# Performance work log

Hardware: AMD Instinct MI355X
Metric: run time of the kernel (lower is better)

Reference implementation:

```python
import jax, jax.numpy as jnp
import numpy as np
import math

B, T, C = 4, 2048, 1024
H, D = 16, 64            # num_heads, head_dim
ORIG_LEN = 4096
MIN_FREQ, MAX_FREQ = 0.5, 40.0


def setup_inputs() -> dict:
    key = jax.random.key(0)
    ks = jax.random.split(key, 6)
    x = jax.random.normal(ks[0], (B, T, C), dtype=jnp.float32)
    keep_idx = jnp.sort(jax.random.randint(ks[1], (B, T, 1), 0, ORIG_LEN), axis=1)
    W_qkv = jax.random.normal(ks[2], (C, 3 * C), dtype=jnp.float32) * (1.0 / math.sqrt(C))
    b_qkv = jnp.zeros((3 * C,), dtype=jnp.float32)
    W_proj = jax.random.normal(ks[3], (C, C), dtype=jnp.float32) * (1.0 / math.sqrt(C))
    b_proj = jnp.zeros((C,), dtype=jnp.float32)
    return {"x": x, "keep_idx": keep_idx, "original_seq_len": ORIG_LEN,
            "W_qkv": W_qkv, "b_qkv": b_qkv, "W_proj": W_proj, "b_proj": b_proj}


def _rope_angles(positions, orig_len):
    # positions: [b, t] float token positions in the ORIGINAL sequence.
    # golden_gate 1-D RoPE: normalized positions times geometric frequency band.
    half = D // 2
    freqs = MIN_FREQ * (MAX_FREQ / MIN_FREQ) ** (jnp.arange(half, dtype=jnp.float32) / (half - 1))
    pos_norm = positions / jnp.float32(orig_len)          # [b, t]
    return 2.0 * jnp.pi * pos_norm[:, :, None] * freqs    # [b, t, half]


def _apply_rope(x, cos, sin):
    # x: [b, h, t, d]; cos/sin: [b, 1, t, d/2]; rotate (first half, second half) pairs
    half = D // 2
    x1, x2 = x[..., :half], x[..., half:]
    return jnp.concatenate([x1 * cos - x2 * sin, x1 * sin + x2 * cos], axis=-1)


def reference(x, keep_idx, original_seq_len, W_qkv, b_qkv, W_proj, b_proj):
    b, t, c = x.shape
    # fused QKV projection + head split: (b,t,3c) -> (b,t,3,h,d) -> (b,h,t,3,d)
    qkv = (x @ W_qkv + b_qkv).reshape(b, t, 3, H, D).transpose(0, 3, 1, 2, 4)
    q, k, v = qkv[:, :, :, 0], qkv[:, :, :, 1], qkv[:, :, :, 2]  # each [b,h,t,d]

    positions = keep_idx[..., 0].astype(jnp.float32)             # [b, t]
    ang = _rope_angles(positions, original_seq_len)              # [b, t, d/2]
    cos = jnp.cos(ang)[:, None]                                  # [b,1,t,d/2]
    sin = jnp.sin(ang)[:, None]
    q = _apply_rope(q, cos, sin)
    k = _apply_rope(k, cos, sin)

    # dense non-causal scaled dot-product attention
    scale = 1.0 / math.sqrt(D)
    scores = jnp.einsum('bhqd,bhkd->bhqk', q, k) * scale
    attn = jax.nn.softmax(scores, axis=-1)
    out = jnp.einsum('bhqk,bhkd->bhqd', attn, v)                 # [b,h,t,d]

    out = out.transpose(0, 2, 1, 3).reshape(b, t, H * D)         # [b,t,c]
    return out @ W_proj + b_proj
```

## Files before the change

### kernel.cpp

```cpp
#include <hip/hip_runtime.h>
#include <hip/hip_bf16.h>
#include <math.h>

#define B_ 4
#define T_ 2048
#define C_ 1024
#define H_ 16
#define D_ 64

typedef __attribute__((ext_vector_type(8))) short bf16x8_t;
typedef __attribute__((ext_vector_type(4))) float f32x4_t;
typedef __attribute__((ext_vector_type(2))) unsigned int uiv2_t;

#define SHIFT2 32.0f

#define GLOAD_LDS16(gp, lp)                                                          \
    __builtin_amdgcn_global_load_lds(                                                \
        (const __attribute__((address_space(1))) void*)(gp),                         \
        (__attribute__((address_space(3))) void*)(lp), 16, 0, 0)

#define WAVE_ORDER() __builtin_amdgcn_wave_barrier()

__device__ inline unsigned int pack2bf(float a, float b) {
    __hip_bfloat162 h = __float22bfloat162_rn(make_float2(a, b));
    return *reinterpret_cast<unsigned int*>(&h);
}

__global__ __launch_bounds__(256)
void prep_kernel(const float* __restrict__ x, __hip_bfloat16* __restrict__ xbf,
                 const int* __restrict__ keep, const int* __restrict__ orig,
                 float* __restrict__ tab,
                 const float* __restrict__ Wqkv, __hip_bfloat16* __restrict__ WqkvT,
                 const float* __restrict__ Wproj, __hip_bfloat16* __restrict__ WprojT) {
    __shared__ float s[32][33];
    const int bid = blockIdx.x;
    const int tid = threadIdx.x;

    if (bid < 8192) {
        int i = bid * 256 + tid;
        float4 v = *(const float4*)(x + (size_t)i * 4);
        uint2 u;
        u.x = pack2bf(v.x, v.y);
        u.y = pack2bf(v.z, v.w);
        *(uint2*)(xbf + (size_t)i * 4) = u;
    } else if (bid < 9216) {
        int i = (bid - 8192) * 256 + tid;
        int tok = i >> 5, d = i & 31;
        float freq = 0.5f * exp2f((float)d * (6.321928094887362f / 31.0f));
        float ang  = 6.283185307179586f * ((float)keep[tok] / (float)(*orig)) * freq;
        tab[(size_t)tok * 64 + d]      = cosf(ang);
        tab[(size_t)tok * 64 + 32 + d] = sinf(ang);
    } else {
        const float* in;
        __hip_bfloat16* outp;
        int N, n0, k0, r;
        if (bid < 12288) {
            r = bid - 9216;
            in = Wqkv; outp = WqkvT; N = 3 * C_;
            n0 = (r % 96) * 32; k0 = (r / 96) * 32;
        } else {
            r = bid - 12288;
            in = Wproj; outp = WprojT; N = C_;
            n0 = (r % 32) * 32; k0 = (r / 32) * 32;
        }
        const int K = C_;
        const int tx = tid & 31;
        const int ty = tid >> 5;
#pragma unroll
        for (int yy = 0; yy < 32; yy += 8)
            s[ty + yy][tx] = in[(size_t)(k0 + ty + yy) * N + n0 + tx];
        __syncthreads();
#pragma unroll
        for (int yy = 0; yy < 32; yy += 8)
            outp[(size_t)(n0 + ty + yy) * K + k0 + tx] = __float2bfloat16(s[tx][ty + yy]);
    }
}

#define GTILE (128 * 32)

template <int MODE>
__global__ __launch_bounds__(256)
void gemm_kernel(const __hip_bfloat16* __restrict__ A,
                 const __hip_bfloat16* __restrict__ BT,
                 const float* __restrict__ bias,
                 float* __restrict__ out,
                 __hip_bfloat16* __restrict__ qbuf,
                 __hip_bfloat16* __restrict__ kbuf,
                 __hip_bfloat16* __restrict__ vtbuf,
                 const float* __restrict__ ropetab,
                 int M, int N, int K) {
    __shared__ __align__(16) __hip_bfloat16 GS[6 * GTILE];

    const int tid  = threadIdx.x;
    const int lane = tid & 63;
    const int wave = tid >> 6;
    const int wm   = wave >> 1;
    const int wn   = wave & 1;
    const int l15  = lane & 15;
    const int quad = lane >> 4;

    const int nT  = N >> 7;
    const int grp = blockIdx.x / (8 * nT);
    const int rem = blockIdx.x - grp * 8 * nT;
    const int m0  = (grp * 8 + (rem & 7)) * 128;
    const int n0  = (rem >> 3) * 128;

    f32x4_t acc[4][4];
#pragma unroll
    for (int i = 0; i < 4; i++)
#pragma unroll
        for (int j = 0; j < 4; j++) acc[i][j] = (f32x4_t)0.0f;

    const int lrow = lane >> 2;
    const int scol = ((lane & 3) ^ ((lane >> 4) & 3)) * 8;
    const __hip_bfloat16* gA  = A  + (size_t)(m0 + wave * 16 + lrow) * K + scol;
    const __hip_bfloat16* gA2 = gA + (size_t)64 * K;
    const __hip_bfloat16* gB  = BT + (size_t)(n0 + wave * 16 + lrow) * K + scol;
    const __hip_bfloat16* gB2 = gB + (size_t)64 * K;
    const int ldsW = wave * 16 * 32;

    const int NK = K >> 5;
    GLOAD_LDS16(gA,  GS + ldsW);
    GLOAD_LDS16(gA2, GS + ldsW + 64 * 32);
    GLOAD_LDS16(gB,  GS + 3 * GTILE + ldsW);
    GLOAD_LDS16(gB2, GS + 3 * GTILE + ldsW + 64 * 32);
    if (NK > 1) {
        GLOAD_LDS16(gA  + 32, GS + GTILE + ldsW);
        GLOAD_LDS16(gA2 + 32, GS + GTILE + ldsW + 64 * 32);
        GLOAD_LDS16(gB  + 32, GS + 3 * GTILE + GTILE + ldsW);
        GLOAD_LDS16(gB2 + 32, GS + 3 * GTILE + GTILE + ldsW + 64 * 32);
    }

    int off = 0;
    for (int t = 0; t < NK; ++t) {
        if (t + 2 < NK) {
            int poff = off + 2 * GTILE;
            if (poff >= 3 * GTILE) poff -= 3 * GTILE;
            const int kk = (t + 2) << 5;
            GLOAD_LDS16(gA  + kk, GS + poff + ldsW);
            GLOAD_LDS16(gA2 + kk, GS + poff + ldsW + 64 * 32);
            GLOAD_LDS16(gB  + kk, GS + 3 * GTILE + poff + ldsW);
            GLOAD_LDS16(gB2 + kk, GS + 3 * GTILE + poff + ldsW + 64 * 32);
            asm volatile("s_waitcnt vmcnt(8)" ::: "memory");
        } else if (t + 1 < NK) {
            asm volatile("s_waitcnt vmcnt(4)" ::: "memory");
        } else {
            asm volatile("s_waitcnt vmcnt(0)" ::: "memory");
        }
        __builtin_amdgcn_s_barrier();
        __builtin_amdgcn_sched_barrier(0);

        bf16x8_t af[4], bfv[4];
#pragma unroll
        for (int i = 0; i < 4; i++)
            af[i] = *(const bf16x8_t*)(GS + off + (wm * 64 + i * 16 + l15) * 32 +
                                       ((quad ^ (l15 >> 2)) * 8));
#pragma unroll
        for (int j = 0; j < 4; j++)
            bfv[j] = *(const bf16x8_t*)(GS + 3 * GTILE + off + (wn * 64 + j * 16 + l15) * 32 +
                                        ((quad ^ (l15 >> 2)) * 8));
#pragma unroll
        for (int i = 0; i < 4; i++)
#pragma unroll
            for (int j = 0; j < 4; j++)
                acc[i][j] = __builtin_amdgcn_mfma_f32_16x16x32_bf16(af[i], bfv[j], acc[i][j], 0, 0, 0);

        __builtin_amdgcn_sched_barrier(0);
        asm volatile("s_waitcnt lgkmcnt(0)" ::: "memory");
        __builtin_amdgcn_s_barrier();

        off += GTILE;
        if (off == 3 * GTILE) off = 0;
    }

    float bv[4];
#pragma unroll
    for (int j = 0; j < 4; j++)
        bv[j] = bias[n0 + wn * 64 + j * 16 + l15];

    if (MODE == 0) {
#pragma unroll
        for (int i = 0; i < 4; i++)
#pragma unroll
            for (int r = 0; r < 4; r++) {
                int row = m0 + wm * 64 + i * 16 + quad * 4 + r;
#pragma unroll
                for (int j = 0; j < 4; j++) {
                    int col = n0 + wn * 64 + j * 16 + l15;
                    out[(size_t)row * N + col] = acc[i][j][r] + bv[j];
                }
            }
    } else {
        const int cb   = n0 + wn * 64;
        const int part = cb >> 10;
        if (part == 2) {
            const int hb = (n0 & 1023) >> 6;
            __hip_bfloat16* myL = GS + wn * (64 * 136);
#pragma unroll
            for (int j = 0; j < 4; j++)
#pragma unroll
                for (int i = 0; i < 4; i++)
#pragma unroll
                    for (int r = 0; r < 4; r++) {
                        int rt = wm * 64 + i * 16 + quad * 4 + r;
                        int d  = j * 16 + l15;
                        myL[d * 136 + rt] = __float2bfloat16(acc[i][j][r] + bv[j]);
                    }
            __syncthreads();
            const int bb  = m0 >> 11;
            const int t0  = m0 & 2047;
            const int row = tid >> 1;
            const int wn2 = row >> 6;
            const int dd  = row & 63;
            const __hip_bfloat16* src = GS + wn2 * (64 * 136) + dd * 136;
            __hip_bfloat16* dstv = vtbuf +
                ((size_t)((bb * H_ + hb + wn2) * D_ + dd)) * T_ + t0;
#pragma unroll
            for (int s2 = 0; s2 < 8; s2++) {
                int ch = (tid & 1) * 8 + s2;
                *(bf16x8_t*)(dstv + ch * 8) = *(const bf16x8_t*)(src + ch * 8);
            }
        } else {
            const int h = (cb & 1023) >> 6;
            __hip_bfloat16* dst = (part == 0) ? qbuf : kbuf;
            const float sc = (part == 0) ? 0.18033688011112042f : 1.0f;
#pragma unroll
            for (int i = 0; i < 4; i++) {
#pragma unroll
                for (int r = 0; r < 4; r++) {
                    int row = m0 + wm * 64 + i * 16 + quad * 4 + r;
                    int b = row >> 11;
                    int t = row & 2047;
                    const float* trow = ropetab + (size_t)row * 64;
                    size_t base = ((size_t)(b * H_ + h) * T_ + t) * D_;
#pragma unroll
                    for (int j = 0; j < 2; j++) {
                        int d = j * 16 + l15;
                        float cs = trow[d];
                        float sn = trow[32 + d];
                        float x1 = acc[i][j][r]     + bv[j];
                        float x2 = acc[i][j + 2][r] + bv[j + 2];
                        dst[base + d]      = __float2bfloat16(sc * (x1 * cs - x2 * sn));
                        dst[base + d + 32] = __float2bfloat16(sc * (x1 * sn + x2 * cs));
                    }
                }
            }
        }
    }
}

#define KVTILE (64 * 64)

__global__ __launch_bounds__(256, 4)
void attn_kernel(const __hip_bfloat16* __restrict__ q,
                 const __hip_bfloat16* __restrict__ k,
                 const __hip_bfloat16* __restrict__ vt,
                 __hip_bfloat16* __restrict__ attn_out) {
    __shared__ __align__(16) __hip_bfloat16 SMEM[4 * KVTILE];

    const int tid  = threadIdx.x;
    const int lane = tid & 63;
    const int wave = tid >> 6;
    const int l15  = lane & 15;
    const int quad = lane >> 4;
    const int x7   = l15 & 7;

    const int bh = blockIdx.x & 63;
    const int qt = blockIdx.x >> 6;
    const int b  = bh >> 4;
    const int h  = bh & 15;

    const size_t qkbase = (size_t)bh * T_ * D_;
    const size_t vbase  = (size_t)bh * D_ * T_;
    const int    qrow0  = qt * 128 + wave * 32;

    const int drow   = lane >> 3;
    const int gchunk = (lane & 7) ^ drow;

    const __hip_bfloat16* kg = k + qkbase;
    const __hip_bfloat16* vg = vt + vbase;

    const int c0 = ((quad)     ^ x7) * 8;
    const int c1 = ((4 + quad) ^ x7) * 8;

    bf16x8_t qa[2][2];
#pragma unroll
    for (int qf = 0; qf < 2; qf++)
#pragma unroll
        for (int kk = 0; kk < 2; kk++)
            qa[qf][kk] = *(const bf16x8_t*)(q + qkbase +
                          (size_t)(qrow0 + qf * 16 + l15) * D_ + kk * 32 + quad * 8);

    bf16x8_t ones;
#pragma unroll
    for (int i = 0; i < 8; i++) ones[i] = (short)0x3F80;

    const f32x4_t mbias = (f32x4_t)(-SHIFT2);

    f32x4_t o[2][4];
#pragma unroll
    for (int qf = 0; qf < 2; qf++)
#pragma unroll
        for (int jd = 0; jd < 4; jd++) o[qf][jd] = (f32x4_t)0.0f;
    f32x4_t osum[2];
    osum[0] = (f32x4_t)0.0f;
    osum[1] = (f32x4_t)0.0f;

#pragma unroll
    for (int i = 0; i < 2; i++) {
        int r = wave * 16 + i * 8;
        GLOAD_LDS16(kg + (size_t)(r + drow) * D_ + gchunk * 8, SMEM + r * 64);
        GLOAD_LDS16(vg + (size_t)(r + drow) * T_ + gchunk * 8, SMEM + 2 * KVTILE + r * 64);
    }

    for (int kt = 0; kt < T_ / 64; kt++) {
        const int curoff = (kt & 1) * KVTILE;
        const int nxtoff = curoff ^ KVTILE;
        if (kt + 1 < T_ / 64) {
#pragma unroll
            for (int i = 0; i < 2; i++) {
                int r = wave * 16 + i * 8;
                GLOAD_LDS16(kg + (size_t)((kt + 1) * 64 + r + drow) * D_ + gchunk * 8,
                            SMEM + nxtoff + r * 64);
                GLOAD_LDS16(vg + (size_t)(r + drow) * T_ + (kt + 1) * 64 + gchunk * 8,
                            SMEM + 2 * KVTILE + nxtoff + r * 64);
            }
            asm volatile("s_waitcnt vmcnt(4)" ::: "memory");
        } else {
            asm volatile("s_waitcnt vmcnt(0)" ::: "memory");
        }
        __builtin_amdgcn_s_barrier();
        __builtin_amdgcn_sched_barrier(0);

        const __hip_bfloat16* KLc = SMEM + curoff;
        const __hip_bfloat16* VLc = SMEM + 2 * KVTILE + curoff;

        bf16x8_t kf[4][2];
#pragma unroll
        for (int jt = 0; jt < 4; jt++) {
            kf[jt][0] = *(const bf16x8_t*)(KLc + (jt * 16 + l15) * 64 + c0);
            kf[jt][1] = *(const bf16x8_t*)(KLc + (jt * 16 + l15) * 64 + c1);
        }

        f32x4_t sT[2][4];
        __builtin_amdgcn_s_setprio(1);
#pragma unroll
        for (int jt = 0; jt < 4; jt++)
#pragma unroll
            for (int qf = 0; qf < 2; qf++) {
                sT[qf][jt] = __builtin_amdgcn_mfma_f32_16x16x32_bf16(
                    kf[jt][0], qa[qf][0], mbias, 0, 0, 0);
                sT[qf][jt] = __builtin_amdgcn_mfma_f32_16x16x32_bf16(
                    kf[jt][1], qa[qf][1], sT[qf][jt], 0, 0, 0);
            }
        __builtin_amdgcn_s_setprio(0);

        bf16x8_t pb[2][2];
#pragma unroll
        for (int qf = 0; qf < 2; qf++) {
            unsigned int w0[4], w1[4];
#pragma unroll
            for (int jt = 0; jt < 4; jt++) {
                float p0 = __builtin_amdgcn_exp2f(sT[qf][jt][0]);
                float p1 = __builtin_amdgcn_exp2f(sT[qf][jt][1]);
                float p2 = __builtin_amdgcn_exp2f(sT[qf][jt][2]);
                float p3 = __builtin_amdgcn_exp2f(sT[qf][jt][3]);
                w0[jt] = pack2bf(p0, p1);
                w1[jt] = pack2bf(p2, p3);
            }
#pragma unroll
            for (int kk = 0; kk < 2; kk++) {
                uiv2_t s0 = __builtin_amdgcn_permlane32_swap(w0[2 * kk], w0[2 * kk + 1], false, false);
                uiv2_t r0 = __builtin_amdgcn_permlane16_swap(s0[0], s0[1], false, false);
                uiv2_t s1 = __builtin_amdgcn_permlane32_swap(w1[2 * kk], w1[2 * kk + 1], false, false);
                uiv2_t r1 = __builtin_amdgcn_permlane16_swap(s1[0], s1[1], false, false);
                union { unsigned int u[4]; bf16x8_t v; } pu;
                pu.u[0] = r0[0];
                pu.u[1] = r1[0];
                pu.u[2] = r0[1];
                pu.u[3] = r1[1];
                pb[qf][kk] = pu.v;
            }
        }

        __builtin_amdgcn_s_setprio(1);
#pragma unroll
        for (int qf = 0; qf < 2; qf++) {
            osum[qf] = __builtin_amdgcn_mfma_f32_16x16x32_bf16(ones, pb[qf][0], osum[qf], 0, 0, 0);
            osum[qf] = __builtin_amdgcn_mfma_f32_16x16x32_bf16(ones, pb[qf][1], osum[qf], 0, 0, 0);
        }

#pragma unroll
        for (int jd = 0; jd < 4; jd++) {
            bf16x8_t vf0 = *(const bf16x8_t*)(VLc + (jd * 16 + l15) * 64 + c0);
            bf16x8_t vf1 = *(const bf16x8_t*)(VLc + (jd * 16 + l15) * 64 + c1);
#pragma unroll
            for (int qf = 0; qf < 2; qf++) {
                o[qf][jd] = __builtin_amdgcn_mfma_f32_16x16x32_bf16(vf0, pb[qf][0], o[qf][jd], 0, 0, 0);
                o[qf][jd] = __builtin_amdgcn_mfma_f32_16x16x32_bf16(vf1, pb[qf][1], o[qf][jd], 0, 0, 0);
            }
        }
        __builtin_amdgcn_s_setprio(0);

        __builtin_amdgcn_sched_barrier(0);
        asm volatile("s_waitcnt lgkmcnt(0)" ::: "memory");
        __builtin_amdgcn_s_barrier();
    }

    float inv[2];
    inv[0] = 1.0f / osum[0][0];
    inv[1] = 1.0f / osum[1][0];

    __hip_bfloat16* Pep = SMEM + wave * (32 * 72);

    WAVE_ORDER();
#pragma unroll
    for (int qf = 0; qf < 2; qf++) {
#pragma unroll
        for (int jd = 0; jd < 4; jd++) {
            uint2 pk;
            pk.x = pack2bf(o[qf][jd][0] * inv[qf], o[qf][jd][1] * inv[qf]);
            pk.y = pack2bf(o[qf][jd][2] * inv[qf], o[qf][jd][3] * inv[qf]);
            *(uint2*)(Pep + (qf * 16 + l15) * 72 + jd * 16 + quad * 4) = pk;
        }
    }
    WAVE_ORDER();

#pragma unroll
    for (int rnd = 0; rnd < 4; rnd++) {
        int row = rnd * 8 + (lane >> 3);
        int col = (lane & 7) * 8;
        bf16x8_t vrow = *(const bf16x8_t*)(Pep + row * 72 + col);
        int token = qt * 128 + wave * 32 + row;
        *(bf16x8_t*)(attn_out + ((size_t)(b * T_ + token)) * C_ + h * 64 + col) = vrow;
    }
}

extern "C" void kernel_launch(void* const* d_in, const int* in_sizes, int n_in,
                              void* d_out, int out_size, void* d_ws, size_t ws_size,
                              hipStream_t stream) {
    const float* x        = (const float*)d_in[0];
    const int*   keep_idx = (const int*)d_in[1];
    const int*   orig_len = (const int*)d_in[2];
    const float* Wqkv     = (const float*)d_in[3];
    const float* bqkv     = (const float*)d_in[4];
    const float* Wproj    = (const float*)d_in[5];
    const float* bproj    = (const float*)d_in[6];
    float*       out      = (float*)d_out;

    const size_t NTOK = (size_t)B_ * T_;
    const size_t QKV1 = NTOK * C_;

    __hip_bfloat16* qbuf    = (__hip_bfloat16*)d_ws;
    __hip_bfloat16* kbuf    = qbuf    + QKV1;
    __hip_bfloat16* vtbuf   = kbuf    + QKV1;
    __hip_bfloat16* attnbuf = vtbuf   + QKV1;
    __hip_bfloat16* WqkvT   = attnbuf + QKV1;
    __hip_bfloat16* WprojT  = WqkvT   + (size_t)C_ * 3 * C_;
    __hip_bfloat16* xbf     = WprojT  + (size_t)C_ * C_;
    float*          ropetab = (float*)(xbf + QKV1);

    prep_kernel<<<13312, 256, 0, stream>>>(x, xbf, keep_idx, orig_len, ropetab,
                                           Wqkv, WqkvT, Wproj, WprojT);

    gemm_kernel<1><<<(8192 / 128) * (3072 / 128), 256, 0, stream>>>(
        xbf, WqkvT, bqkv, nullptr, qbuf, kbuf, vtbuf, ropetab, 8192, 3072, 1024);

    attn_kernel<<<(T_ / 128) * 64, 256, 0, stream>>>(qbuf, kbuf, vtbuf, attnbuf);

    gemm_kernel<0><<<(8192 / 128) * (1024 / 128), 256, 0, stream>>>(
        attnbuf, WprojT, bproj, out, nullptr, nullptr, nullptr, nullptr, 8192, 1024, 1024);
}
```

Before: 273.6 us.

## Enlarge GEMM tile to 256x128 with 8 waves and double buffering

Both GEMMs now use 256x128 output tiles computed by 512-thread blocks (8 waves) instead of 128x128 with 4 waves. This halves the grid and the B-operand reloads per output element. The LDS pipeline changes from a 3-stage ring with two tiles in flight to a 2-stage double buffer with one prefetch. The V-transpose epilogue is reworked to write packed pairs and emit the 256-row tile in two 128-row passes through LDS. The cost is less prefetch depth and fewer, larger blocks, which could hurt latency hiding and occupancy.

```diff
diff --git a/kernel.cpp b/kernel.cpp
--- a/kernel.cpp
+++ b/kernel.cpp
@@ -76,10 +76,11 @@
     }
 }
 
-#define GTILE (128 * 32)
+#define ATILE (256 * 32)
+#define BTILE (128 * 32)
 
 template <int MODE>
-__global__ __launch_bounds__(256)
+__global__ __launch_bounds__(512)
 void gemm_kernel(const __hip_bfloat16* __restrict__ A,
                  const __hip_bfloat16* __restrict__ BT,
                  const float* __restrict__ bias,
@@ -89,7 +90,7 @@
                  __hip_bfloat16* __restrict__ vtbuf,
                  const float* __restrict__ ropetab,
                  int M, int N, int K) {
-    __shared__ __align__(16) __hip_bfloat16 GS[6 * GTILE];
+    __shared__ __align__(16) __hip_bfloat16 GS[2 * ATILE + 2 * BTILE];
 
     const int tid  = threadIdx.x;
     const int lane = tid & 63;
@@ -102,7 +103,7 @@
     const int nT  = N >> 7;
     const int grp = blockIdx.x / (8 * nT);
     const int rem = blockIdx.x - grp * 8 * nT;
-    const int m0  = (grp * 8 + (rem & 7)) * 128;
+    const int m0  = (grp * 8 + (rem & 7)) * 256;
     const int n0  = (rem >> 3) * 128;
 
     f32x4_t acc[4][4];
@@ -113,37 +114,28 @@
 
     const int lrow = lane >> 2;
     const int scol = ((lane & 3) ^ ((lane >> 4) & 3)) * 8;
-    const __hip_bfloat16* gA  = A  + (size_t)(m0 + wave * 16 + lrow) * K + scol;
-    const __hip_bfloat16* gA2 = gA + (size_t)64 * K;
+    const __hip_bfloat16* gA  = A  + (size_t)(m0 + wave * 32 + lrow) * K + scol;
+    const __hip_bfloat16* gA2 = gA + (size_t)16 * K;
     const __hip_bfloat16* gB  = BT + (size_t)(n0 + wave * 16 + lrow) * K + scol;
-    const __hip_bfloat16* gB2 = gB + (size_t)64 * K;
-    const int ldsW = wave * 16 * 32;
+    const int ldsA = wave * 32 * 32;
+    const int ldsB = wave * 16 * 32;
 
     const int NK = K >> 5;
-    GLOAD_LDS16(gA,  GS + ldsW);
-    GLOAD_LDS16(gA2, GS + ldsW + 64 * 32);
-    GLOAD_LDS16(gB,  GS + 3 * GTILE + ldsW);
-    GLOAD_LDS16(gB2, GS + 3 * GTILE + ldsW + 64 * 32);
-    if (NK > 1) {
-        GLOAD_LDS16(gA  + 32, GS + GTILE + ldsW);
-        GLOAD_LDS16(gA2 + 32, GS + GTILE + ldsW + 64 * 32);
-        GLOAD_LDS16(gB  + 32, GS + 3 * GTILE + GTILE + ldsW);
-        GLOAD_LDS16(gB2 + 32, GS + 3 * GTILE + GTILE + ldsW + 64 * 32);
-    }
-
-    int off = 0;
+    GLOAD_LDS16(gA,  GS + ldsA);
+    GLOAD_LDS16(gA2, GS + ldsA + 16 * 32);
+    GLOAD_LDS16(gB,  GS + 2 * ATILE + ldsB);
+
     for (int t = 0; t < NK; ++t) {
-        if (t + 2 < NK) {
-            int poff = off + 2 * GTILE;
-            if (poff >= 3 * GTILE) poff -= 3 * GTILE;
-            const int kk = (t + 2) << 5;
-            GLOAD_LDS16(gA  + kk, GS + poff + ldsW);
-            GLOAD_LDS16(gA2 + kk, GS + poff + ldsW + 64 * 32);
-            GLOAD_LDS16(gB  + kk, GS + 3 * GTILE + poff + ldsW);
-            GLOAD_LDS16(gB2 + kk, GS + 3 * GTILE + poff + ldsW + 64 * 32);
-            asm volatile("s_waitcnt vmcnt(8)" ::: "memory");
-        } else if (t + 1 < NK) {
-            asm volatile("s_waitcnt vmcnt(4)" ::: "memory");
+        const int Ab = (t & 1) * ATILE;
+        const int Bb = 2 * ATILE + (t & 1) * BTILE;
+        if (t + 1 < NK) {
+            const int An = (~t & 1) * ATILE;
+            const int Bn = 2 * ATILE + (~t & 1) * BTILE;
+            const int kk = (t + 1) << 5;
+            GLOAD_LDS16(gA  + kk, GS + An + ldsA);
+            GLOAD_LDS16(gA2 + kk, GS + An + ldsA + 16 * 32);
+            GLOAD_LDS16(gB  + kk, GS + Bn + ldsB);
+            asm volatile("s_waitcnt vmcnt(3)" ::: "memory");
         } else {
             asm volatile("s_waitcnt vmcnt(0)" ::: "memory");
         }
@@ -153,11 +145,11 @@
         bf16x8_t af[4], bfv[4];
 #pragma unroll
         for (int i = 0; i < 4; i++)
-            af[i] = *(const bf16x8_t*)(GS + off + (wm * 64 + i * 16 + l15) * 32 +
+            af[i] = *(const bf16x8_t*)(GS + Ab + (wm * 64 + i * 16 + l15) * 32 +
                                        ((quad ^ (l15 >> 2)) * 8));
 #pragma unroll
         for (int j = 0; j < 4; j++)
-            bfv[j] = *(const bf16x8_t*)(GS + 3 * GTILE + off + (wn * 64 + j * 16 + l15) * 32 +
+            bfv[j] = *(const bf16x8_t*)(GS + Bb + (wn * 64 + j * 16 + l15) * 32 +
                                         ((quad ^ (l15 >> 2)) * 8));
 #pragma unroll
         for (int i = 0; i < 4; i++)
@@ -168,9 +160,6 @@
         __builtin_amdgcn_sched_barrier(0);
         asm volatile("s_waitcnt lgkmcnt(0)" ::: "memory");
         __builtin_amdgcn_s_barrier();
-
-        off += GTILE;
-        if (off == 3 * GTILE) off = 0;
     }
 
     float bv[4];
@@ -195,30 +184,40 @@
         const int part = cb >> 10;
         if (part == 2) {
             const int hb = (n0 & 1023) >> 6;
-            __hip_bfloat16* myL = GS + wn * (64 * 136);
-#pragma unroll
-            for (int j = 0; j < 4; j++)
-#pragma unroll
-                for (int i = 0; i < 4; i++)
-#pragma unroll
-                    for (int r = 0; r < 4; r++) {
-                        int rt = wm * 64 + i * 16 + quad * 4 + r;
-                        int d  = j * 16 + l15;
-                        myL[d * 136 + rt] = __float2bfloat16(acc[i][j][r] + bv[j]);
+            const int bb = m0 >> 11;
+            const int t0 = m0 & 2047;
+            __hip_bfloat16* L = GS;
+#pragma unroll
+            for (int p = 0; p < 2; ++p) {
+                if ((wm >> 1) == p) {
+#pragma unroll
+                    for (int j = 0; j < 4; j++) {
+                        int d = wn * 64 + j * 16 + l15;
+#pragma unroll
+                        for (int i = 0; i < 4; i++) {
+                            int rtb = (wm & 1) * 64 + i * 16 + quad * 4;
+                            uint2 pk;
+                            pk.x = pack2bf(acc[i][j][0] + bv[j], acc[i][j][1] + bv[j]);
+                            pk.y = pack2bf(acc[i][j][2] + bv[j], acc[i][j][3] + bv[j]);
+                            *(uint2*)(L + d * 136 + rtb) = pk;
+                        }
                     }
-            __syncthreads();
-            const int bb  = m0 >> 11;
-            const int t0  = m0 & 2047;
-            const int row = tid >> 1;
-            const int wn2 = row >> 6;
-            const int dd  = row & 63;
-            const __hip_bfloat16* src = GS + wn2 * (64 * 136) + dd * 136;
-            __hip_bfloat16* dstv = vtbuf +
-                ((size_t)((bb * H_ + hb + wn2) * D_ + dd)) * T_ + t0;
-#pragma unroll
-            for (int s2 = 0; s2 < 8; s2++) {
-                int ch = (tid & 1) * 8 + s2;
-                *(bf16x8_t*)(dstv + ch * 8) = *(const bf16x8_t*)(src + ch * 8);
+                }
+                __syncthreads();
+                {
+                    int row = tid >> 2;
+                    int hb2 = hb + (row >> 6);
+                    int dd  = row & 63;
+                    const __hip_bfloat16* src = L + row * 136;
+                    __hip_bfloat16* dstv = vtbuf +
+                        ((size_t)((bb * H_ + hb2) * D_ + dd)) * T_ + t0 + p * 128;
+#pragma unroll
+                    for (int s2 = 0; s2 < 4; s2++) {
+                        int ch = (tid & 3) + s2 * 4;
+                        *(bf16x8_t*)(dstv + ch * 8) = *(const bf16x8_t*)(src + ch * 8);
+                    }
+                }
+                if (p == 0) __syncthreads();
             }
         } else {
             const int h = (cb & 1023) >> 6;
@@ -463,11 +462,11 @@
     prep_kernel<<<13312, 256, 0, stream>>>(x, xbf, keep_idx, orig_len, ropetab,
                                            Wqkv, WqkvT, Wproj, WprojT);
 
-    gemm_kernel<1><<<(8192 / 128) * (3072 / 128), 256, 0, stream>>>(
+    gemm_kernel<1><<<(8192 / 256) * (3072 / 128), 512, 0, stream>>>(
         xbf, WqkvT, bqkv, nullptr, qbuf, kbuf, vtbuf, ropetab, 8192, 3072, 1024);
 
     attn_kernel<<<(T_ / 128) * 64, 256, 0, stream>>>(qbuf, kbuf, vtbuf, attnbuf);
 
-    gemm_kernel<0><<<(8192 / 128) * (1024 / 128), 256, 0, stream>>>(
+    gemm_kernel<0><<<(8192 / 256) * (1024 / 128), 512, 0, stream>>>(
         attnbuf, WprojT, bproj, out, nullptr, nullptr, nullptr, nullptr, 8192, 1024, 1024);
 }
```

Measured after the change: 269.2 us. About the same (-1.6%).
